# Kernel optimization log

Measured on AMD Instinct MI355X. Metric: run time of the kernel, lower is better.

The kernel has to match this reference:

```python
import jax, jax.numpy as jnp
import numpy as np

HIDDEN = 128
GRID = 8
NEIGH = 4.0
CELL = NEIGH / GRID


def setup_inputs() -> dict:
    key = jax.random.key(0)
    k1, k2, k3, k4 = jax.random.split(key, 4)
    B, N = 64, 64
    hidden_states = jax.random.normal(k1, (B, N, HIDDEN), dtype=jnp.float32)
    positions = jax.random.normal(k2, (B, N, 2), dtype=jnp.float32)
    fan_in = HIDDEN * GRID * GRID
    bound = 1.0 / np.sqrt(fan_in)
    W = jax.random.uniform(k3, (HIDDEN, fan_in), minval=-bound, maxval=bound, dtype=jnp.float32)
    b = jax.random.uniform(k4, (HIDDEN,), minval=-bound, maxval=bound, dtype=jnp.float32)
    return {"hidden_states": hidden_states, "positions": positions, "W": W, "b": b}


def reference(hidden_states, positions, W, b):
    B, N, H = hidden_states.shape
    G, G2 = GRID, GRID * GRID
    # rel[b, i, j] = positions[b, j] - positions[b, i]  (offset of neighbor j in agent i's frame)
    rel = positions[:, None, :, :] - positions[:, :, None, :]  # [B, N, N, 2]
    # torch .long() truncates toward zero; jnp astype(int32) does the same, and after
    # clamping to [0, G-1] this matches the original exactly.
    gx = ((rel[..., 0] + NEIGH / 2) / CELL).astype(jnp.int32).clip(0, G - 1)
    gy = ((rel[..., 1] + NEIGH / 2) / CELL).astype(jnp.int32).clip(0, G - 1)
    cell = gx * G + gy  # [B, N(i), N(j)] flat grid-cell index (gx-major, matching view order)
    # Exclude self (j == i) from pooling.
    not_self = (1.0 - jnp.eye(N, dtype=hidden_states.dtype))  # [N(i), N(j)]
    onehot = jax.nn.one_hot(cell, G2, dtype=hidden_states.dtype) * not_self[None, :, :, None]
    # Scatter-add neighbor hidden states into each agent's grid: [B, N(i), G2, H]
    grid = jnp.einsum('bijc,bjh->bich', onehot, hidden_states)
    grid_flat = grid.reshape(B, N, G2 * H)  # (gx, gy, h) flatten order == torch .view
    pooled = grid_flat @ W.T + b  # [B, N, H]
    return pooled
```

## Files before the change

### kernel.cpp

```cpp
#include <hip/hip_runtime.h>
#include <hip/hip_bf16.h>
#include <stdint.h>


typedef __attribute__((ext_vector_type(8))) short bf16x8;
typedef __attribute__((ext_vector_type(4))) float f32x4;

#define NCHUNK 8
#define CPB 8

__device__ inline void load_lds16(const void* g, void* l) {
    __builtin_amdgcn_global_load_lds(
        (const __attribute__((address_space(1))) unsigned int*)g,
        (__attribute__((address_space(3))) unsigned int*)l, 16, 0, 0);
}

__device__ inline unsigned short bf16bits(float x) {
    __hip_bfloat16 h = __float2bfloat16(x);
    return *reinterpret_cast<unsigned short*>(&h);
}

__global__ __launch_bounds__(512)
void gp_wconv(const float* __restrict__ W, __hip_bfloat16* __restrict__ Wb)
{
    __shared__ __attribute__((aligned(16))) __hip_bfloat16 Wl[128][136];
    const int c = blockIdx.x, t = threadIdx.x;
    #pragma unroll
    for (int q = 0; q < 8; ++q) {
        int flat = q * 512 + t;
        int ho = flat >> 5, k4 = flat & 31;
        float4 v = *(const float4*)(W + (size_t)ho * 8192 + c * 128 + k4 * 4);
        __hip_bfloat16* d = &Wl[ho][k4 * 4];
        d[0] = __float2bfloat16(v.x); d[1] = __float2bfloat16(v.y);
        d[2] = __float2bfloat16(v.z); d[3] = __float2bfloat16(v.w);
    }
    __syncthreads();
    #pragma unroll
    for (int q = 0; q < 4; ++q) {
        int flat = q * 512 + t;
        int hg = flat >> 7, ho = flat & 127;
        bf16x8 v = *(const bf16x8*)&Wl[ho][hg * 8];
        *(bf16x8*)(Wb + (size_t)c * 16384 + (size_t)flat * 8) = v;
    }
}

__global__ __launch_bounds__(512, 4)
void gp_main(const float* __restrict__ hid, const float* __restrict__ pos,
             const __hip_bfloat16* __restrict__ Wb, float* __restrict__ partial)
{
    __shared__ __attribute__((aligned(16))) __hip_bfloat16 Ws[16 * 128 * 8];
    __shared__ __attribute__((aligned(16))) __hip_bfloat16 Hs[16 * 64 * 8];
    __shared__ __attribute__((aligned(16))) __hip_bfloat16 Zt[8 * 128 * 8];
    __shared__ __attribute__((aligned(16))) __hip_bfloat16 Ms[8 * 64 * 8];
    __shared__ unsigned char cellt[64 * 64];
    __shared__ float ps[128];

    const int t = threadIdx.x;
    const int b = blockIdx.x & 63, chunk = blockIdx.x >> 6;
    const int w = t >> 6, lane = t & 63;
    const int l15 = lane & 15, kg = lane >> 4;
    const int mw = w & 1, nw = w >> 1;

    if (t < 128) ps[t] = pos[(size_t)b * 128 + t];
    __syncthreads();

    #pragma unroll
    for (int q = 0; q < 8; ++q) {
        int idx = q * 512 + t;
        int i = idx >> 6, j = idx & 63;
        float rx = ps[j * 2 + 0] - ps[i * 2 + 0];
        float ry = ps[j * 2 + 1] - ps[i * 2 + 1];
        int gx = (int)((rx + 2.0f) * 2.0f);
        int gy = (int)((ry + 2.0f) * 2.0f);
        gx = gx < 0 ? 0 : (gx > 7 ? 7 : gx);
        gy = gy < 0 ? 0 : (gy > 7 ? 7 : gy);
        cellt[idx] = (i == j) ? 255 : (unsigned char)(gx * 8 + gy);
    }
    #pragma unroll
    for (int q = 0; q < 2; ++q) {
        int idx = q * 512 + t;
        int hg = idx >> 6, j = idx & 63;
        const float* src = hid + ((size_t)b * 64 + j) * 128 + hg * 8;
        float4 v0 = *(const float4*)src;
        float4 v1 = *(const float4*)(src + 4);
        __hip_bfloat16* d = &Hs[(hg * 64 + j) * 8];
        d[0] = __float2bfloat16(v0.x); d[1] = __float2bfloat16(v0.y);
        d[2] = __float2bfloat16(v0.z); d[3] = __float2bfloat16(v0.w);
        d[4] = __float2bfloat16(v1.x); d[5] = __float2bfloat16(v1.y);
        d[6] = __float2bfloat16(v1.z); d[7] = __float2bfloat16(v1.w);
    }

    f32x4 acc[2][2];
    #pragma unroll
    for (int fm = 0; fm < 2; ++fm)
        #pragma unroll
        for (int fn = 0; fn < 2; ++fn)
            acc[fm][fn] = (f32x4){0.f, 0.f, 0.f, 0.f};

    for (int cc = 0; cc < CPB; ++cc) {
        const int c = chunk * CPB + cc;
        __syncthreads();
        const char* gsrc = (const char*)(Wb + (size_t)c * 16384);
        #pragma unroll
        for (int r = 0; r < 4; ++r) {
            int off = r * 8192 + w * 1024 + lane * 16;
            load_lds16(gsrc + off, (char*)Ws + off);
        }
        {
            int i = t & 63, jg = t >> 6;
            const unsigned char* cr = &cellt[i * 64 + jg * 8];
            __hip_bfloat16* d = &Ms[(jg * 64 + i) * 8];
            #pragma unroll
            for (int e = 0; e < 8; ++e)
                d[e] = __float2bfloat16(cr[e] == c ? 1.0f : 0.0f);
        }
        __syncthreads();

        f32x4 z[2][2];
        #pragma unroll
        for (int fm = 0; fm < 2; ++fm)
            #pragma unroll
            for (int fn = 0; fn < 2; ++fn)
                z[fm][fn] = (f32x4){0.f, 0.f, 0.f, 0.f};
        #pragma unroll
        for (int ks = 0; ks < 4; ++ks) {
            int hg = ks * 4 + kg;
            bf16x8 a0 = *(const bf16x8*)&Hs[(hg * 64 + mw * 32 + l15) * 8];
            bf16x8 a1 = *(const bf16x8*)&Hs[(hg * 64 + mw * 32 + 16 + l15) * 8];
            bf16x8 b0 = *(const bf16x8*)&Ws[(hg * 128 + nw * 32 + l15) * 8];
            bf16x8 b1 = *(const bf16x8*)&Ws[(hg * 128 + nw * 32 + 16 + l15) * 8];
            z[0][0] = __builtin_amdgcn_mfma_f32_16x16x32_bf16(a0, b0, z[0][0], 0, 0, 0);
            z[0][1] = __builtin_amdgcn_mfma_f32_16x16x32_bf16(a0, b1, z[0][1], 0, 0, 0);
            z[1][0] = __builtin_amdgcn_mfma_f32_16x16x32_bf16(a1, b0, z[1][0], 0, 0, 0);
            z[1][1] = __builtin_amdgcn_mfma_f32_16x16x32_bf16(a1, b1, z[1][1], 0, 0, 0);
        }
        #pragma unroll
        for (int fm = 0; fm < 2; ++fm) {
            #pragma unroll
            for (int fn = 0; fn < 2; ++fn) {
                int j0 = mw * 32 + fm * 16 + kg * 4;
                int jg = j0 >> 3, e0 = j0 & 7;
                int ho = nw * 32 + fn * 16 + l15;
                union { unsigned short us[4]; uint2 v; } pk;
                pk.us[0] = bf16bits(z[fm][fn][0]);
                pk.us[1] = bf16bits(z[fm][fn][1]);
                pk.us[2] = bf16bits(z[fm][fn][2]);
                pk.us[3] = bf16bits(z[fm][fn][3]);
                *(uint2*)((char*)Zt + ((size_t)(jg * 128 + ho) * 8 + e0) * 2) = pk.v;
            }
        }
        __syncthreads();

        #pragma unroll
        for (int ks = 0; ks < 2; ++ks) {
            int jg = ks * 4 + kg;
            bf16x8 a0 = *(const bf16x8*)&Ms[(jg * 64 + mw * 32 + l15) * 8];
            bf16x8 a1 = *(const bf16x8*)&Ms[(jg * 64 + mw * 32 + 16 + l15) * 8];
            bf16x8 b0 = *(const bf16x8*)&Zt[(jg * 128 + nw * 32 + l15) * 8];
            bf16x8 b1 = *(const bf16x8*)&Zt[(jg * 128 + nw * 32 + 16 + l15) * 8];
            acc[0][0] = __builtin_amdgcn_mfma_f32_16x16x32_bf16(a0, b0, acc[0][0], 0, 0, 0);
            acc[0][1] = __builtin_amdgcn_mfma_f32_16x16x32_bf16(a0, b1, acc[0][1], 0, 0, 0);
            acc[1][0] = __builtin_amdgcn_mfma_f32_16x16x32_bf16(a1, b0, acc[1][0], 0, 0, 0);
            acc[1][1] = __builtin_amdgcn_mfma_f32_16x16x32_bf16(a1, b1, acc[1][1], 0, 0, 0);
        }
    }

    float* pb = partial + (((size_t)chunk * 64 + b) * 64) * 128;
    #pragma unroll
    for (int fm = 0; fm < 2; ++fm)
        #pragma unroll
        for (int fn = 0; fn < 2; ++fn)
            #pragma unroll
            for (int r = 0; r < 4; ++r) {
                int i = mw * 32 + fm * 16 + kg * 4 + r;
                int ho = nw * 32 + fn * 16 + l15;
                pb[(size_t)i * 128 + ho] = acc[fm][fn][r];
            }
}

__global__ __launch_bounds__(512)
void gp_reduce(const float* __restrict__ partial, const float* __restrict__ bias,
               float* __restrict__ out)
{
    int gid = blockIdx.x * 512 + threadIdx.x;
    int ho4 = gid & 31;
    float4 a = *(const float4*)(bias + ho4 * 4);
    #pragma unroll
    for (int ch = 0; ch < NCHUNK; ++ch) {
        float4 v = *(const float4*)(partial + (size_t)ch * 524288 + (size_t)gid * 4);
        a.x += v.x; a.y += v.y; a.z += v.z; a.w += v.w;
    }
    *(float4*)(out + (size_t)gid * 4) = a;
}

extern "C" void kernel_launch(void* const* d_in, const int* in_sizes, int n_in,
                              void* d_out, int out_size, void* d_ws, size_t ws_size,
                              hipStream_t stream)
{
    const float* hid  = (const float*)d_in[0];
    const float* pos  = (const float*)d_in[1];
    const float* W    = (const float*)d_in[2];
    const float* bias = (const float*)d_in[3];
    float* out = (float*)d_out;

    __hip_bfloat16* Wb = (__hip_bfloat16*)d_ws;
    float* partial = (float*)((char*)d_ws + (size_t)2097152);

    hipLaunchKernelGGL(gp_wconv,  dim3(64),         dim3(512), 0, stream, W, Wb);
    hipLaunchKernelGGL(gp_main,   dim3(NCHUNK * 64), dim3(512), 0, stream, hid, pos, Wb, partial);
    hipLaunchKernelGGL(gp_reduce, dim3(256),        dim3(512), 0, stream, partial, bias, out);
}
```

Before: 35.51 us.

## Load W fragments directly to registers and double-buffer Zt/Ms to drop barriers

Replaces the per-chunk global_load_lds staging of the W tile with direct global loads into MFMA B-fragment registers, and hoists the hidden-state A fragments into registers once before the loop. Zt and Ms become double-buffered by chunk parity, so two of the three __syncthreads per iteration go away and the loop is unrolled by two. This aims to cut barrier stalls and LDS traffic. The cost is more VGPR pressure at launch_bounds(512,4) and uncoalesced, LDS-less global reads of W that each wave reissues.

```diff
diff --git a/kernel.cpp b/kernel.cpp
--- a/kernel.cpp
+++ b/kernel.cpp
@@ -8,12 +8,6 @@
 
 #define NCHUNK 8
 #define CPB 8
-
-__device__ inline void load_lds16(const void* g, void* l) {
-    __builtin_amdgcn_global_load_lds(
-        (const __attribute__((address_space(1))) unsigned int*)g,
-        (__attribute__((address_space(3))) unsigned int*)l, 16, 0, 0);
-}
 
 __device__ inline unsigned short bf16bits(float x) {
     __hip_bfloat16 h = __float2bfloat16(x);
@@ -48,10 +42,9 @@
 void gp_main(const float* __restrict__ hid, const float* __restrict__ pos,
              const __hip_bfloat16* __restrict__ Wb, float* __restrict__ partial)
 {
-    __shared__ __attribute__((aligned(16))) __hip_bfloat16 Ws[16 * 128 * 8];
     __shared__ __attribute__((aligned(16))) __hip_bfloat16 Hs[16 * 64 * 8];
-    __shared__ __attribute__((aligned(16))) __hip_bfloat16 Zt[8 * 128 * 8];
-    __shared__ __attribute__((aligned(16))) __hip_bfloat16 Ms[8 * 64 * 8];
+    __shared__ __attribute__((aligned(16))) __hip_bfloat16 Zt[2][8 * 128 * 8];
+    __shared__ __attribute__((aligned(16))) __hip_bfloat16 Ms[2][8 * 64 * 8];
     __shared__ unsigned char cellt[64 * 64];
     __shared__ float ps[128];
 
@@ -89,6 +82,15 @@
         d[4] = __float2bfloat16(v1.x); d[5] = __float2bfloat16(v1.y);
         d[6] = __float2bfloat16(v1.z); d[7] = __float2bfloat16(v1.w);
     }
+    __syncthreads();
+
+    bf16x8 afr[2][4];
+    #pragma unroll
+    for (int ks = 0; ks < 4; ++ks) {
+        int hg = ks * 4 + kg;
+        afr[0][ks] = *(const bf16x8*)&Hs[(hg * 64 + mw * 32 + l15) * 8];
+        afr[1][ks] = *(const bf16x8*)&Hs[(hg * 64 + mw * 32 + 16 + l15) * 8];
+    }
 
     f32x4 acc[2][2];
     #pragma unroll
@@ -97,24 +99,28 @@
         for (int fn = 0; fn < 2; ++fn)
             acc[fm][fn] = (f32x4){0.f, 0.f, 0.f, 0.f};
 
+    #pragma unroll 2
     for (int cc = 0; cc < CPB; ++cc) {
+        const int p = cc & 1;
         const int c = chunk * CPB + cc;
-        __syncthreads();
-        const char* gsrc = (const char*)(Wb + (size_t)c * 16384);
-        #pragma unroll
-        for (int r = 0; r < 4; ++r) {
-            int off = r * 8192 + w * 1024 + lane * 16;
-            load_lds16(gsrc + off, (char*)Ws + off);
-        }
+
+        const __hip_bfloat16* wc = Wb + (size_t)c * 16384;
+        bf16x8 bfr[4][2];
+        #pragma unroll
+        for (int ks = 0; ks < 4; ++ks) {
+            int hg = ks * 4 + kg;
+            bfr[ks][0] = *(const bf16x8*)(wc + ((size_t)hg * 128 + nw * 32 + l15) * 8);
+            bfr[ks][1] = *(const bf16x8*)(wc + ((size_t)hg * 128 + nw * 32 + 16 + l15) * 8);
+        }
+
         {
             int i = t & 63, jg = t >> 6;
             const unsigned char* cr = &cellt[i * 64 + jg * 8];
-            __hip_bfloat16* d = &Ms[(jg * 64 + i) * 8];
+            __hip_bfloat16* d = &Ms[p][(jg * 64 + i) * 8];
             #pragma unroll
             for (int e = 0; e < 8; ++e)
                 d[e] = __float2bfloat16(cr[e] == c ? 1.0f : 0.0f);
         }
-        __syncthreads();
 
         f32x4 z[2][2];
         #pragma unroll
@@ -124,16 +130,12 @@
                 z[fm][fn] = (f32x4){0.f, 0.f, 0.f, 0.f};
         #pragma unroll
         for (int ks = 0; ks < 4; ++ks) {
-            int hg = ks * 4 + kg;
-            bf16x8 a0 = *(const bf16x8*)&Hs[(hg * 64 + mw * 32 + l15) * 8];
-            bf16x8 a1 = *(const bf16x8*)&Hs[(hg * 64 + mw * 32 + 16 + l15) * 8];
-            bf16x8 b0 = *(const bf16x8*)&Ws[(hg * 128 + nw * 32 + l15) * 8];
-            bf16x8 b1 = *(const bf16x8*)&Ws[(hg * 128 + nw * 32 + 16 + l15) * 8];
-            z[0][0] = __builtin_amdgcn_mfma_f32_16x16x32_bf16(a0, b0, z[0][0], 0, 0, 0);
-            z[0][1] = __builtin_amdgcn_mfma_f32_16x16x32_bf16(a0, b1, z[0][1], 0, 0, 0);
-            z[1][0] = __builtin_amdgcn_mfma_f32_16x16x32_bf16(a1, b0, z[1][0], 0, 0, 0);
-            z[1][1] = __builtin_amdgcn_mfma_f32_16x16x32_bf16(a1, b1, z[1][1], 0, 0, 0);
-        }
+            z[0][0] = __builtin_amdgcn_mfma_f32_16x16x32_bf16(afr[0][ks], bfr[ks][0], z[0][0], 0, 0, 0);
+            z[0][1] = __builtin_amdgcn_mfma_f32_16x16x32_bf16(afr[0][ks], bfr[ks][1], z[0][1], 0, 0, 0);
+            z[1][0] = __builtin_amdgcn_mfma_f32_16x16x32_bf16(afr[1][ks], bfr[ks][0], z[1][0], 0, 0, 0);
+            z[1][1] = __builtin_amdgcn_mfma_f32_16x16x32_bf16(afr[1][ks], bfr[ks][1], z[1][1], 0, 0, 0);
+        }
+
         #pragma unroll
         for (int fm = 0; fm < 2; ++fm) {
             #pragma unroll
@@ -146,7 +148,7 @@
                 pk.us[1] = bf16bits(z[fm][fn][1]);
                 pk.us[2] = bf16bits(z[fm][fn][2]);
                 pk.us[3] = bf16bits(z[fm][fn][3]);
-                *(uint2*)((char*)Zt + ((size_t)(jg * 128 + ho) * 8 + e0) * 2) = pk.v;
+                *(uint2*)((char*)&Zt[p][0] + ((size_t)(jg * 128 + ho) * 8 + e0) * 2) = pk.v;
             }
         }
         __syncthreads();
@@ -154,10 +156,10 @@
         #pragma unroll
         for (int ks = 0; ks < 2; ++ks) {
             int jg = ks * 4 + kg;
-            bf16x8 a0 = *(const bf16x8*)&Ms[(jg * 64 + mw * 32 + l15) * 8];
-            bf16x8 a1 = *(const bf16x8*)&Ms[(jg * 64 + mw * 32 + 16 + l15) * 8];
-            bf16x8 b0 = *(const bf16x8*)&Zt[(jg * 128 + nw * 32 + l15) * 8];
-            bf16x8 b1 = *(const bf16x8*)&Zt[(jg * 128 + nw * 32 + 16 + l15) * 8];
+            bf16x8 a0 = *(const bf16x8*)&Ms[p][(jg * 64 + mw * 32 + l15) * 8];
+            bf16x8 a1 = *(const bf16x8*)&Ms[p][(jg * 64 + mw * 32 + 16 + l15) * 8];
+            bf16x8 b0 = *(const bf16x8*)&Zt[p][(jg * 128 + nw * 32 + l15) * 8];
+            bf16x8 b1 = *(const bf16x8*)&Zt[p][(jg * 128 + nw * 32 + 16 + l15) * 8];
             acc[0][0] = __builtin_amdgcn_mfma_f32_16x16x32_bf16(a0, b0, acc[0][0], 0, 0, 0);
             acc[0][1] = __builtin_amdgcn_mfma_f32_16x16x32_bf16(a0, b1, acc[0][1], 0, 0, 0);
             acc[1][0] = __builtin_amdgcn_mfma_f32_16x16x32_bf16(a1, b0, acc[1][0], 0, 0, 0);
@@ -206,7 +208,7 @@
     __hip_bfloat16* Wb = (__hip_bfloat16*)d_ws;
     float* partial = (float*)((char*)d_ws + (size_t)2097152);
 
-    hipLaunchKernelGGL(gp_wconv,  dim3(64),         dim3(512), 0, stream, W, Wb);
+    hipLaunchKernelGGL(gp_wconv,  dim3(64),          dim3(512), 0, stream, W, Wb);
     hipLaunchKernelGGL(gp_main,   dim3(NCHUNK * 64), dim3(512), 0, stream, hid, pos, Wb, partial);
-    hipLaunchKernelGGL(gp_reduce, dim3(256),        dim3(512), 0, stream, partial, bias, out);
-}
+    hipLaunchKernelGGL(gp_reduce, dim3(256),         dim3(512), 0, stream, partial, bias, out);
+}
```

Result: faster. 34.25 us (-3.5%).
